# Performance work log

Measured on AMD Instinct MI355X. Metric: run time of the kernel, lower is better.

The kernel has to match this reference:

```python
import jax, jax.numpy as jnp
import numpy as np

B, N_IN, N_OUT, N_NODES, N_EDGES = 64, 128, 256, 20000, 320000
ITERS, LEAK, IN_AMP, OUT_AMP = 150, 0.01, 1.2, 1.2


def setup_inputs() -> dict:
    key = jax.random.key(0)
    ks = jax.random.split(key, 8)
    x = jax.random.normal(ks[0], (B, N_IN), dtype=jnp.float32)
    # projection weights (inputAmplitude / projectionAmplitude * ones)
    in_w = IN_AMP * jnp.ones((N_IN,), dtype=jnp.float32)
    out_w = OUT_AMP * jnp.ones((N_OUT,), dtype=jnp.float32)
    rec_w = 0.1 + 0.1 * jax.random.uniform(ks[1], (N_EDGES,), dtype=jnp.float32)
    inhib = jax.random.bernoulli(ks[2], 0.3, (N_EDGES,))
    rec_w = jnp.where(inhib, -rec_w, rec_w)
    biases = 0.001 * jnp.ones((N_NODES, 1), dtype=jnp.float32)
    rows = jax.random.randint(ks[3], (N_EDGES,), 0, N_NODES)
    cols = jax.random.randint(ks[4], (N_EDGES,), 0, N_NODES)
    in_idx = jax.random.randint(ks[5], (N_IN,), 0, N_NODES)
    out_idx = jax.random.randint(ks[6], (N_OUT,), 0, N_NODES)
    return {"x": x, "in_w": in_w, "out_w": out_w, "rec_w": rec_w,
            "biases": biases, "rows": rows, "cols": cols,
            "in_idx": in_idx, "out_idx": out_idx}


def reference(x, in_w, out_w, rec_w, biases, rows, cols, in_idx, out_idx):
    n_nodes = biases.shape[0]

    def mml_act(v):
        # leaky below 0, Michaelis-Menten-like saturation above 0.5
        v = jnp.where(v < 0, v * LEAK, v)
        return jnp.where(v > 0.5, 1.0 - 0.25 / v, v)

    def spmv(h):
        # A @ h with A in COO form: out[r] += w_e * h[c]
        msg = rec_w[:, None] * h[cols]                      # [E, B]
        return jax.ops.segment_sum(msg, rows, num_segments=n_nodes)

    # input projection: scatter weighted inputs into node vector
    y = jnp.zeros((x.shape[0], n_nodes), x.dtype).at[:, in_idx].set(in_w * x)
    b_in = y.T + biases                                      # [N, B]

    def step(h, _):
        return mml_act(spmv(h) + b_in), None

    h0 = jnp.zeros_like(b_in)
    hT, _ = jax.lax.scan(step, h0, None, length=ITERS)
    xhat = hT.T                                              # [B, N]
    return out_w * xhat[:, out_idx]                          # [B, n_out]
```

## Files before the change

kernel.cpp:

```cpp
#include <hip/hip_runtime.h>
#include <hip/hip_fp16.h>

#define N_NODES 20000
#define N_EDGES 320000
#define BATCH   64
#define N_IN    128
#define N_OUT   256
#define CAP     64
#define ITERS   150
#define LEAK    0.01f

#define CNT_MASK 0x3FFFFFFF
#define FLAG_BIT (1 << 30)

#define NSLICE 32
#define BPS    8
#define NPB    2500
#define NT     1024
#define NBLK   (NSLICE * BPS)
#define SLICE_U32 20480
#define OWN_U128  625
#define PAIRS  32
#define TAG_STRIDE 32

typedef unsigned int uint;
typedef unsigned long long ull;
typedef _Float16 h2_t __attribute__((ext_vector_type(2)));
typedef uint u32x4 __attribute__((ext_vector_type(4)));

__device__ __forceinline__ void st128_mall(u32x4* p, u32x4 v) {
    asm volatile("global_store_dwordx4 %0, %1, off sc0 sc1"
                 :: "v"(p), "v"(v) : "memory");
}
__device__ __forceinline__ void st32_mall(uint* p, uint v) {
    asm volatile("global_store_dword %0, %1, off sc0 sc1"
                 :: "v"(p), "v"(v) : "memory");
}
__device__ __forceinline__ uint ld32_mall(const uint* p) {
    uint v;
    asm volatile("global_load_dword %0, %1, off sc0 sc1\n\t"
                 "s_waitcnt vmcnt(0)"
                 : "=v"(v) : "v"(p) : "memory");
    return v;
}

__device__ __forceinline__ float fdot2u(uint w, uint h, float acc) {
    union { uint u; h2_t h; } a, b; a.u = w; b.u = h;
    return __builtin_amdgcn_fdot2(a.h, b.h, acc, false);
}

__global__ void setup_kernel(uint* __restrict__ hGA, uint* __restrict__ hGB,
                             int* __restrict__ cnt,
                             uint* __restrict__ colpair, uint* __restrict__ wpair,
                             uint* __restrict__ tags) {
    int idx = blockIdx.x * blockDim.x + threadIdx.x;
    int stride = gridDim.x * blockDim.x;
    for (int i = idx; i < NSLICE * SLICE_U32; i += stride) { hGA[i] = 0u; hGB[i] = 0u; }
    for (int i = idx; i < N_NODES; i += stride) cnt[i] = 0;
    for (int i = idx; i < PAIRS * N_NODES; i += stride) { colpair[i] = 0u; wpair[i] = 0u; }
    for (int i = idx; i < NSLICE * BPS * TAG_STRIDE; i += stride) tags[i] = 0u;
}

__global__ void input_scatter_kernel(float* __restrict__ bin,
                                     const float* __restrict__ x,
                                     const float* __restrict__ in_w,
                                     const int* __restrict__ in_idx,
                                     const float* __restrict__ biases,
                                     int* __restrict__ cnt) {
    int i = blockIdx.x;
    int b = threadIdx.x;
    int node = in_idx[i];
    if (b == 0) atomicOr(&cnt[node], FLAG_BIT);
    for (int j = i + 1; j < N_IN; j++)
        if (in_idx[j] == node) return;
    bin[node * BATCH + b] = biases[node] + in_w[i] * x[b * N_IN + i];
}

__global__ void ell_build_kernel(const int* __restrict__ rows,
                                 const int* __restrict__ cols,
                                 const float* __restrict__ rec_w,
                                 uint* __restrict__ colpair, uint* __restrict__ wpair,
                                 int* __restrict__ cnt) {
    int e = blockIdx.x * blockDim.x + threadIdx.x;
    if (e >= N_EDGES) return;
    int r = rows[e];
    int s = atomicAdd(&cnt[r], 1) & CNT_MASK;
    if (s < CAP) {
        int p = s >> 1, sh = (s & 1) * 16;
        atomicOr(&colpair[(size_t)p * N_NODES + r], (uint)cols[e] << sh);
        uint hw = (uint)__half_as_ushort(__float2half(rec_w[e]));
        atomicOr(&wpair[(size_t)p * N_NODES + r], hw << sh);
    }
}

__global__ __launch_bounds__(NT) void sort_kernel(const int* __restrict__ cnt,
                                                  int* __restrict__ permG,
                                                  int* __restrict__ rankOf) {
    __shared__ int hist[65], off[65];
    int nbase = blockIdx.x * NPB;
    int tid = threadIdx.x;
    if (tid < 65) hist[tid] = 0;
    __syncthreads();
    for (int r = tid; r < NPB; r += NT) {
        int c = cnt[nbase + r] & CNT_MASK; if (c > CAP) c = CAP;
        atomicAdd(&hist[c], 1);
    }
    __syncthreads();
    if (tid == 0) {
        int run = 0;
        for (int c = CAP; c >= 0; c--) { off[c] = run; run += hist[c]; }
    }
    __syncthreads();
    for (int r = tid; r < NPB; r += NT) {
        int c = cnt[nbase + r] & CNT_MASK; if (c > CAP) c = CAP;
        int rk = atomicAdd(&off[c], 1);
        permG[nbase + rk] = nbase + r;
        rankOf[nbase + r] = nbase + rk;
    }
}

__global__ void reorder_kernel(const uint* __restrict__ colpair,
                               const uint* __restrict__ wpair,
                               const int* __restrict__ permG,
                               const int* __restrict__ rankOf,
                               uint2* __restrict__ cwR) {
    int r = blockIdx.x * blockDim.x + threadIdx.x;
    int p = blockIdx.y;
    if (r >= N_NODES) return;
    size_t o = (size_t)p * N_NODES;
    int n = permG[r];
    uint cc = colpair[o + n];
    uint lo = (uint)rankOf[cc & 0xFFFFu];
    uint hi = (uint)rankOf[cc >> 16];
    cwR[o + r] = make_uint2(lo | (hi << 16), wpair[o + n]);
}

__device__ __forceinline__ uint finish_node(float a0, float a1, float b0, float b1) {
    float r0 = b0 + a0, r1 = b1 + a1;
    float u0 = (r0 < 0.f) ? r0 * LEAK : r0;
    float u1 = (r1 < 0.f) ? r1 * LEAK : r1;
    float v0 = (u0 > 0.5f) ? (1.0f - 0.25f / u0) : u0;
    float v1 = (u1 > 0.5f) ? (1.0f - 0.25f / u1) : u1;
    union { __half2 h; uint u; } p;
    p.h = __halves2half2(__float2half(v0), __float2half(v1));
    return p.u;
}

__device__ __forceinline__ void hoist_consts(
        int nbase, int tid, int s,
        const int* __restrict__ cnt, const int* __restrict__ permG,
        const float* __restrict__ bin, const float* __restrict__ biases,
        int* rank, float* mb0, float* mb1, bool* ma, int& kp) {
    int kmax = 0;
#pragma unroll
    for (int j = 0; j < 3; j++) {
        int sl = 3 * tid + j;
        ma[j] = (sl < NPB);
        rank[j] = nbase + (ma[j] ? sl : 0);
        int n = permG[rank[j]];
        int cv = cnt[n];
        int c = cv & CNT_MASK; if (c > CAP) c = CAP;
        if (ma[j] && c > kmax) kmax = c;
        if (cv & FLAG_BIT) {
            mb0[j] = bin[(size_t)n * BATCH + 2 * s];
            mb1[j] = bin[(size_t)n * BATCH + 2 * s + 1];
        } else {
            float bb = biases[n]; mb0[j] = bb; mb1[j] = bb;
        }
    }
    kp = (kmax + 1) >> 1;
}

__device__ __forceinline__ void compute_pairs(
        const int* rank, int kp,
        const uint2* __restrict__ cwR,
        const uint* __restrict__ lds_h, float* a0, float* a1) {
    a0[0] = a0[1] = a0[2] = 0.f;
    a1[0] = a1[1] = a1[2] = 0.f;
#pragma unroll 2
    for (int p = 0; p < kp; p++) {
        size_t o = (size_t)p * N_NODES;
#pragma unroll
        for (int j = 0; j < 3; j++) {
            uint2 m = cwR[o + rank[j]];
            uint ha = lds_h[m.x & 0xFFFFu];
            uint hb = lds_h[m.x >> 16];
            uint lo = __builtin_amdgcn_perm(hb, ha, 0x05040100u);
            uint hi = __builtin_amdgcn_perm(hb, ha, 0x07060302u);
            a0[j] = fdot2u(m.y, lo, a0[j]);
            a1[j] = fdot2u(m.y, hi, a1[j]);
        }
    }
}

__global__ __launch_bounds__(NT) void persistent_kernel(
        uint* hGA, uint* hGB,
        const float* __restrict__ bin, const float* __restrict__ biases,
        const uint2* __restrict__ cwR,
        const int* __restrict__ cnt, const int* __restrict__ permG,
        uint* tags) {
    extern __shared__ uint lds_all[];
    uint* bufA = lds_all;
    uint* bufB = lds_all + SLICE_U32;
    int bid = blockIdx.x, tid = threadIdx.x;
    int s = bid >> 3, sub = bid & 7;
    int nbase = sub * NPB;
    const int wave = tid >> 6, lane = tid & 63;

    int rank[3]; float mb0[3], mb1[3]; bool ma[3]; int kp;
    hoist_consts(nbase, tid, s, cnt, permG, bin, biases, rank, mb0, mb1, ma, kp);

    for (int i = tid; i < SLICE_U32; i += NT) bufA[i] = 0u;
    __syncthreads();

    uint* hA_s = hGA + (size_t)s * SLICE_U32;
    uint* hB_s = hGB + (size_t)s * SLICE_U32;
    uint* mytag = &tags[(s * BPS + sub) * TAG_STRIDE];

    uint* cur = bufA;
    uint* nxt = bufB;

    for (int t = 0; t < ITERS; t++) {
        uint* hout = (t & 1) ? hB_s : hA_s;

        float a0[3], a1[3];
        compute_pairs(rank, kp, cwR, cur, a0, a1);
#pragma unroll
        for (int j = 0; j < 3; j++)
            if (ma[j]) nxt[rank[j]] = finish_node(a0[j], a1[j], mb0[j], mb1[j]);

        __syncthreads();
        if (tid < OWN_U128) {
            int i = sub * OWN_U128 + tid;
            st128_mall((u32x4*)hout + i, ((const u32x4*)nxt)[i]);
        }
        if (t == ITERS - 1) break;

        __syncthreads();
        if (tid == 0) st32_mall(mytag, (uint)(t + 1));

        if (wave < 14) {
            int sb_idx = wave >> 1;
            int sb = sb_idx + (sb_idx >= sub ? 1 : 0);
            int half = wave & 1;
            if (lane == 0) {
                const uint* rt = &tags[(s * BPS + sb) * TAG_STRIDE];
                while (ld32_mall(rt) < (uint)(t + 1)) __builtin_amdgcn_s_sleep(2);
            }
            const u32x4* sp = (const u32x4*)hout + sb * OWN_U128;
            u32x4* dp = (u32x4*)nxt + sb * OWN_U128;
            int it0 = half * 64 + lane;
            int it4 = it0 + 512;
            int c4 = (it4 <= 624) ? it4 : 624;
            u32x4 r0, r1, r2, r3, r4;
            asm volatile(
                "global_load_dwordx4 %0, %5, off sc0 sc1\n\t"
                "global_load_dwordx4 %1, %6, off sc0 sc1\n\t"
                "global_load_dwordx4 %2, %7, off sc0 sc1\n\t"
                "global_load_dwordx4 %3, %8, off sc0 sc1\n\t"
                "global_load_dwordx4 %4, %9, off sc0 sc1\n\t"
                "s_waitcnt vmcnt(0)"
                : "=&v"(r0), "=&v"(r1), "=&v"(r2), "=&v"(r3), "=&v"(r4)
                : "v"(sp + it0), "v"(sp + it0 + 128), "v"(sp + it0 + 256),
                  "v"(sp + it0 + 384), "v"(sp + c4)
                : "memory");
            dp[it0] = r0; dp[it0 + 128] = r1; dp[it0 + 256] = r2;
            dp[it0 + 384] = r3;
            if (it4 <= 624) dp[it4] = r4;
        }
        __syncthreads();
        uint* tmp = cur; cur = nxt; nxt = tmp;
    }
}

__global__ __launch_bounds__(NT) void step_kernel(
        const uint* __restrict__ hprev, uint* __restrict__ hnext,
        const float* __restrict__ bin, const float* __restrict__ biases,
        const uint2* __restrict__ cwR,
        const int* __restrict__ cnt, const int* __restrict__ permG) {
    extern __shared__ uint lds_h[];
    int bid = blockIdx.x, tid = threadIdx.x;
    int s = bid >> 3, sub = bid & 7;
    int nbase = sub * NPB;

    int rank[3]; float mb0[3], mb1[3]; bool ma[3]; int kp;
    hoist_consts(nbase, tid, s, cnt, permG, bin, biases, rank, mb0, mb1, ma, kp);

    const uint* hp = hprev + (size_t)s * SLICE_U32;
    for (int i = tid; i < SLICE_U32; i += NT) lds_h[i] = hp[i];
    __syncthreads();

    float a0[3], a1[3];
    compute_pairs(rank, kp, cwR, lds_h, a0, a1);
    uint* ho = hnext + (size_t)s * SLICE_U32;
#pragma unroll
    for (int j = 0; j < 3; j++)
        if (ma[j]) ho[rank[j]] = finish_node(a0[j], a1[j], mb0[j], mb1[j]);
}

__global__ void output_kernel(const uint* __restrict__ hfinal,
                              const int* __restrict__ out_idx,
                              const int* __restrict__ rankOf,
                              const float* __restrict__ out_w,
                              float* __restrict__ out) {
    int o = threadIdx.x;
    int b = blockIdx.x;
    uint v = hfinal[(size_t)(b >> 1) * SLICE_U32 + rankOf[out_idx[o]]];
    unsigned short h = (b & 1) ? (unsigned short)(v >> 16) : (unsigned short)(v & 0xFFFF);
    out[b * N_OUT + o] = out_w[o] * __half2float(__ushort_as_half(h));
}

extern "C" void kernel_launch(void* const* d_in, const int* in_sizes, int n_in,
                              void* d_out, int out_size, void* d_ws, size_t ws_size,
                              hipStream_t stream) {
    const float* x      = (const float*)d_in[0];
    const float* in_w   = (const float*)d_in[1];
    const float* out_w  = (const float*)d_in[2];
    const float* rec_w  = (const float*)d_in[3];
    const float* biases = (const float*)d_in[4];
    const int*   rows   = (const int*)d_in[5];
    const int*   cols   = (const int*)d_in[6];
    const int*   in_idx = (const int*)d_in[7];
    const int*   oidx   = (const int*)d_in[8];
    float* out = (float*)d_out;

    char* ws = (char*)d_ws;
    uint*  hGA     = (uint*)ws;  ws += (size_t)NSLICE * SLICE_U32 * 4;
    uint*  hGB     = (uint*)ws;  ws += (size_t)NSLICE * SLICE_U32 * 4;
    float* bin     = (float*)ws; ws += (size_t)N_NODES * BATCH * 4;
    uint*  colpair = (uint*)ws;  ws += (size_t)PAIRS * N_NODES * 4;
    uint*  wpair   = (uint*)ws;  ws += (size_t)PAIRS * N_NODES * 4;
    uint2* cwR     = (uint2*)ws; ws += (size_t)PAIRS * N_NODES * 8;
    int*   cnt     = (int*)ws;   ws += (size_t)N_NODES * 4;
    int*   permG   = (int*)ws;   ws += (size_t)N_NODES * 4;
    int*   rankOf  = (int*)ws;   ws += (size_t)N_NODES * 4;
    uint*  tags    = (uint*)ws;  ws += (size_t)NSLICE * BPS * TAG_STRIDE * 4;

    const int shmem_p = 2 * SLICE_U32 * 4;
    const int shmem_f = SLICE_U32 * 4;
    hipFuncSetAttribute((const void*)persistent_kernel,
                        hipFuncAttributeMaxDynamicSharedMemorySize, shmem_p);
    hipFuncSetAttribute((const void*)step_kernel,
                        hipFuncAttributeMaxDynamicSharedMemorySize, shmem_f);

    setup_kernel<<<2048, 256, 0, stream>>>(hGA, hGB, cnt, colpair, wpair, tags);
    input_scatter_kernel<<<N_IN, BATCH, 0, stream>>>(bin, x, in_w, in_idx,
                                                     biases, cnt);
    ell_build_kernel<<<(N_EDGES + 255) / 256, 256, 0, stream>>>(rows, cols, rec_w,
                                                                colpair, wpair, cnt);
    sort_kernel<<<N_NODES / NPB, NT, 0, stream>>>(cnt, permG, rankOf);
    reorder_kernel<<<dim3((N_NODES + 255) / 256, PAIRS), 256, 0, stream>>>(
        colpair, wpair, permG, rankOf, cwR);

    void* args[] = { (void*)&hGA, (void*)&hGB, (void*)&bin, (void*)&biases,
                     (void*)&cwR, (void*)&cnt, (void*)&permG, (void*)&tags };
    hipError_t ce = hipLaunchCooperativeKernel((void*)persistent_kernel,
                                               dim3(NBLK), dim3(NT),
                                               args, shmem_p, stream);
    const uint* hfinal;
    if (ce == hipSuccess) {
        hfinal = hGB;
    } else {
        uint* pa = hGA;
        uint* pb = hGB;
        for (int t = 0; t < ITERS; t++) {
            step_kernel<<<NBLK, NT, shmem_f, stream>>>(pa, pb, bin, biases,
                                                       cwR, cnt, permG);
            uint* tmp = pa; pa = pb; pb = tmp;
        }
        hfinal = pa;
    }

    output_kernel<<<BATCH, N_OUT, 0, stream>>>(hfinal, oidx, rankOf, out_w, out);
}
```

Measured before the change: 1.048 ms.

## Assign four nodes per thread and use per-wave chunk flags for halo exchange

Each active thread (625 of 1024) now computes four consecutive ranked nodes and writes them as one 128-bit store to both LDS and global memory. This removes the block-wide barrier before publishing. Block-level tags are replaced by per-wave chunk tags (10 chunks per block). Consumer waves poll and copy individual 64-vector chunks from peer blocks as soon as each is ready, which gives finer-grained producer/consumer overlap. The cost is fewer active threads during compute, more tag polling traffic, and 70 chunk waits spread across 16 waves.

```diff
diff --git a/kernel.cpp b/kernel.cpp
--- a/kernel.cpp
+++ b/kernel.cpp
@@ -19,8 +19,9 @@
 #define NT     1024
 #define NBLK   (NSLICE * BPS)
 #define SLICE_U32 20480
-#define OWN_U128  625
 #define PAIRS  32
+#define ACT    625
+#define NWCH   10
 #define TAG_STRIDE 32
 
 typedef unsigned int uint;
@@ -31,6 +32,13 @@
 __device__ __forceinline__ void st128_mall(u32x4* p, u32x4 v) {
     asm volatile("global_store_dwordx4 %0, %1, off sc0 sc1"
                  :: "v"(p), "v"(v) : "memory");
+}
+__device__ __forceinline__ u32x4 ld128_mall(const u32x4* p) {
+    u32x4 v;
+    asm volatile("global_load_dwordx4 %0, %1, off sc0 sc1\n\t"
+                 "s_waitcnt vmcnt(0)"
+                 : "=v"(v) : "v"(p) : "memory");
+    return v;
 }
 __device__ __forceinline__ void st32_mall(uint* p, uint v) {
     asm volatile("global_store_dword %0, %1, off sc0 sc1"
@@ -58,7 +66,7 @@
     for (int i = idx; i < NSLICE * SLICE_U32; i += stride) { hGA[i] = 0u; hGB[i] = 0u; }
     for (int i = idx; i < N_NODES; i += stride) cnt[i] = 0;
     for (int i = idx; i < PAIRS * N_NODES; i += stride) { colpair[i] = 0u; wpair[i] = 0u; }
-    for (int i = idx; i < NSLICE * BPS * TAG_STRIDE; i += stride) tags[i] = 0u;
+    for (int i = idx; i < NSLICE * BPS * NWCH * TAG_STRIDE; i += stride) tags[i] = 0u;
 }
 
 __global__ void input_scatter_kernel(float* __restrict__ bin,
@@ -146,21 +154,19 @@
     return p.u;
 }
 
-__device__ __forceinline__ void hoist_consts(
+__device__ __forceinline__ void hoist4(
         int nbase, int tid, int s,
         const int* __restrict__ cnt, const int* __restrict__ permG,
         const float* __restrict__ bin, const float* __restrict__ biases,
-        int* rank, float* mb0, float* mb1, bool* ma, int& kp) {
+        int& rb, float* mb0, float* mb1, int& kp) {
+    rb = nbase + 4 * tid;
     int kmax = 0;
 #pragma unroll
-    for (int j = 0; j < 3; j++) {
-        int sl = 3 * tid + j;
-        ma[j] = (sl < NPB);
-        rank[j] = nbase + (ma[j] ? sl : 0);
-        int n = permG[rank[j]];
+    for (int j = 0; j < 4; j++) {
+        int n = permG[rb + j];
         int cv = cnt[n];
         int c = cv & CNT_MASK; if (c > CAP) c = CAP;
-        if (ma[j] && c > kmax) kmax = c;
+        if (c > kmax) kmax = c;
         if (cv & FLAG_BIT) {
             mb0[j] = bin[(size_t)n * BATCH + 2 * s];
             mb1[j] = bin[(size_t)n * BATCH + 2 * s + 1];
@@ -171,18 +177,17 @@
     kp = (kmax + 1) >> 1;
 }
 
-__device__ __forceinline__ void compute_pairs(
-        const int* rank, int kp,
-        const uint2* __restrict__ cwR,
+__device__ __forceinline__ void compute4(
+        int rb, int kp, const uint2* __restrict__ cwR,
         const uint* __restrict__ lds_h, float* a0, float* a1) {
-    a0[0] = a0[1] = a0[2] = 0.f;
-    a1[0] = a1[1] = a1[2] = 0.f;
+#pragma unroll
+    for (int j = 0; j < 4; j++) { a0[j] = 0.f; a1[j] = 0.f; }
 #pragma unroll 2
     for (int p = 0; p < kp; p++) {
         size_t o = (size_t)p * N_NODES;
 #pragma unroll
-        for (int j = 0; j < 3; j++) {
-            uint2 m = cwR[o + rank[j]];
+        for (int j = 0; j < 4; j++) {
+            uint2 m = cwR[o + rb + j];
             uint ha = lds_h[m.x & 0xFFFFu];
             uint hb = lds_h[m.x >> 16];
             uint lo = __builtin_amdgcn_perm(hb, ha, 0x05040100u);
@@ -206,16 +211,16 @@
     int s = bid >> 3, sub = bid & 7;
     int nbase = sub * NPB;
     const int wave = tid >> 6, lane = tid & 63;
-
-    int rank[3]; float mb0[3], mb1[3]; bool ma[3]; int kp;
-    hoist_consts(nbase, tid, s, cnt, permG, bin, biases, rank, mb0, mb1, ma, kp);
+    const bool act = (tid < ACT);
+
+    int rb = 0, kp = 0; float mb0[4], mb1[4];
+    if (act) hoist4(nbase, tid, s, cnt, permG, bin, biases, rb, mb0, mb1, kp);
 
     for (int i = tid; i < SLICE_U32; i += NT) bufA[i] = 0u;
     __syncthreads();
 
     uint* hA_s = hGA + (size_t)s * SLICE_U32;
     uint* hB_s = hGB + (size_t)s * SLICE_U32;
-    uint* mytag = &tags[(s * BPS + sub) * TAG_STRIDE];
 
     uint* cur = bufA;
     uint* nxt = bufB;
@@ -223,51 +228,43 @@
     for (int t = 0; t < ITERS; t++) {
         uint* hout = (t & 1) ? hB_s : hA_s;
 
-        float a0[3], a1[3];
-        compute_pairs(rank, kp, cwR, cur, a0, a1);
-#pragma unroll
-        for (int j = 0; j < 3; j++)
-            if (ma[j]) nxt[rank[j]] = finish_node(a0[j], a1[j], mb0[j], mb1[j]);
-
-        __syncthreads();
-        if (tid < OWN_U128) {
-            int i = sub * OWN_U128 + tid;
-            st128_mall((u32x4*)hout + i, ((const u32x4*)nxt)[i]);
+        if (act) {
+            float a0[4], a1[4];
+            compute4(rb, kp, cwR, cur, a0, a1);
+            u32x4 pv;
+            pv.x = finish_node(a0[0], a1[0], mb0[0], mb1[0]);
+            pv.y = finish_node(a0[1], a1[1], mb0[1], mb1[1]);
+            pv.z = finish_node(a0[2], a1[2], mb0[2], mb1[2]);
+            pv.w = finish_node(a0[3], a1[3], mb0[3], mb1[3]);
+            int i4 = rb >> 2;
+            ((u32x4*)nxt)[i4] = pv;
+            st128_mall((u32x4*)hout + i4, pv);
         }
         if (t == ITERS - 1) break;
 
-        __syncthreads();
-        if (tid == 0) st32_mall(mytag, (uint)(t + 1));
-
-        if (wave < 14) {
-            int sb_idx = wave >> 1;
-            int sb = sb_idx + (sb_idx >= sub ? 1 : 0);
-            int half = wave & 1;
+        if (wave < NWCH) {
+            asm volatile("s_waitcnt vmcnt(0)" ::: "memory");
+            if (lane == 0)
+                st32_mall(&tags[((s * BPS + sub) * NWCH + wave) * TAG_STRIDE],
+                          (uint)(t + 1));
+        }
+
+        for (int c = 15 - wave; c < 7 * NWCH; c += 16) {
+            int sub_idx = c / NWCH;
+            int sb = sub_idx + (sub_idx >= sub ? 1 : 0);
+            int wch = c % NWCH;
+            const uint* rt = &tags[((s * BPS + sb) * NWCH + wch) * TAG_STRIDE];
             if (lane == 0) {
-                const uint* rt = &tags[(s * BPS + sb) * TAG_STRIDE];
                 while (ld32_mall(rt) < (uint)(t + 1)) __builtin_amdgcn_s_sleep(2);
             }
-            const u32x4* sp = (const u32x4*)hout + sb * OWN_U128;
-            u32x4* dp = (u32x4*)nxt + sb * OWN_U128;
-            int it0 = half * 64 + lane;
-            int it4 = it0 + 512;
-            int c4 = (it4 <= 624) ? it4 : 624;
-            u32x4 r0, r1, r2, r3, r4;
-            asm volatile(
-                "global_load_dwordx4 %0, %5, off sc0 sc1\n\t"
-                "global_load_dwordx4 %1, %6, off sc0 sc1\n\t"
-                "global_load_dwordx4 %2, %7, off sc0 sc1\n\t"
-                "global_load_dwordx4 %3, %8, off sc0 sc1\n\t"
-                "global_load_dwordx4 %4, %9, off sc0 sc1\n\t"
-                "s_waitcnt vmcnt(0)"
-                : "=&v"(r0), "=&v"(r1), "=&v"(r2), "=&v"(r3), "=&v"(r4)
-                : "v"(sp + it0), "v"(sp + it0 + 128), "v"(sp + it0 + 256),
-                  "v"(sp + it0 + 384), "v"(sp + c4)
-                : "memory");
-            dp[it0] = r0; dp[it0 + 128] = r1; dp[it0 + 256] = r2;
-            dp[it0 + 384] = r3;
-            if (it4 <= 624) dp[it4] = r4;
-        }
+            int n4 = (wch == 9) ? 49 : 64;
+            if (lane < n4) {
+                int idx4 = sb * (NPB / 4) + wch * 64 + lane;
+                u32x4 v = ld128_mall((const u32x4*)hout + idx4);
+                ((u32x4*)nxt)[idx4] = v;
+            }
+        }
+
         __syncthreads();
         uint* tmp = cur; cur = nxt; nxt = tmp;
     }
@@ -283,19 +280,23 @@
     int s = bid >> 3, sub = bid & 7;
     int nbase = sub * NPB;
 
-    int rank[3]; float mb0[3], mb1[3]; bool ma[3]; int kp;
-    hoist_consts(nbase, tid, s, cnt, permG, bin, biases, rank, mb0, mb1, ma, kp);
+    int rb = 0, kp = 0; float mb0[4], mb1[4];
+    if (tid < ACT) hoist4(nbase, tid, s, cnt, permG, bin, biases, rb, mb0, mb1, kp);
 
     const uint* hp = hprev + (size_t)s * SLICE_U32;
     for (int i = tid; i < SLICE_U32; i += NT) lds_h[i] = hp[i];
     __syncthreads();
 
-    float a0[3], a1[3];
-    compute_pairs(rank, kp, cwR, lds_h, a0, a1);
-    uint* ho = hnext + (size_t)s * SLICE_U32;
-#pragma unroll
-    for (int j = 0; j < 3; j++)
-        if (ma[j]) ho[rank[j]] = finish_node(a0[j], a1[j], mb0[j], mb1[j]);
+    if (tid < ACT) {
+        float a0[4], a1[4];
+        compute4(rb, kp, cwR, lds_h, a0, a1);
+        u32x4 pv;
+        pv.x = finish_node(a0[0], a1[0], mb0[0], mb1[0]);
+        pv.y = finish_node(a0[1], a1[1], mb0[1], mb1[1]);
+        pv.z = finish_node(a0[2], a1[2], mb0[2], mb1[2]);
+        pv.w = finish_node(a0[3], a1[3], mb0[3], mb1[3]);
+        ((u32x4*)(hnext + (size_t)s * SLICE_U32))[rb >> 2] = pv;
+    }
 }
 
 __global__ void output_kernel(const uint* __restrict__ hfinal,
@@ -334,7 +335,7 @@
     int*   cnt     = (int*)ws;   ws += (size_t)N_NODES * 4;
     int*   permG   = (int*)ws;   ws += (size_t)N_NODES * 4;
     int*   rankOf  = (int*)ws;   ws += (size_t)N_NODES * 4;
-    uint*  tags    = (uint*)ws;  ws += (size_t)NSLICE * BPS * TAG_STRIDE * 4;
+    uint*  tags    = (uint*)ws;  ws += (size_t)NSLICE * BPS * NWCH * TAG_STRIDE * 4;
 
     const int shmem_p = 2 * SLICE_U32 * 4;
     const int shmem_f = SLICE_U32 * 4;
```

Result: slower. 1.435 ms (+36.9%).
